# Optimization experiments

Hardware: AMD Instinct MI355X
Metric: run time of the kernel (lower is better)

Reference implementation:

```python
import jax, jax.numpy as jnp
import numpy as np

EPS = 1e-5

def _ln(t, g, b):
    m = t.mean(-1, keepdims=True)
    v = ((t - m) ** 2).mean(-1, keepdims=True)
    return (t - m) * jax.lax.rsqrt(v + EPS) * g + b

def _sr(t, w, b, H, W, sr):
    # t: [B, H*W, C] -> spatial-reduction conv -> [B, (H//sr)*(W//sr), C]
    B, L, C = t.shape
    xi = t.transpose(0, 2, 1).reshape(B, C, H, W)
    y = jax.lax.conv_general_dilated(xi, w, (sr, sr), 'VALID',
                                     dimension_numbers=('NCHW', 'OIHW', 'NCHW'))
    return y.reshape(B, C, -1).transpose(0, 2, 1) + b

def setup_inputs() -> dict:
    key = jax.random.key(0)
    ks = jax.random.split(key, 9)
    C, head, sr, H, W = 128, 2, 2, 64, 64
    B, N = 4, 2 * H * W
    s = 0.02
    return {
        'x': jax.random.normal(ks[0], (B, N, C), jnp.float32),
        'qW': jax.random.normal(ks[1], (C, C), jnp.float32) * s,
        'qb': jnp.zeros((C,), jnp.float32),
        'kvW': jax.random.normal(ks[2], (C, 2 * C), jnp.float32) * s,
        'kvb': jnp.zeros((2 * C,), jnp.float32),
        'projW': jax.random.normal(ks[3], (C, C), jnp.float32) * s,
        'projb': jnp.zeros((C,), jnp.float32),
        'srW': jax.random.normal(ks[4], (C, C, sr, sr), jnp.float32) * s,
        'srb': jnp.zeros((C,), jnp.float32),
        'lnW': jnp.ones((C,), jnp.float32),
        'lnB': jnp.zeros((C,), jnp.float32),
        'H': H, 'W': W, 'fuse': 1,
    }

def reference(x, qW, qb, kvW, kvb, projW, projb, srW, srb, lnW, lnB, H, W, fuse):
    head, sr = 2, 2
    B, N, C = x.shape
    Dh = C // head
    scale = Dh ** -0.5
    q = (x @ qW + qb).reshape(B, N, head, Dh).transpose(0, 2, 1, 3)  # [B,h,N,Dh]
    mask = None
    if fuse and sr > 1:
        half = N // 2
        x_rgb = _ln(_sr(x[:, :half, :], srW, srb, H, W, sr), lnW, lnB)
        x_dte = _ln(_sr(x[:, half:, :], srW, srb, H, W, sr), lnW, lnB)
        xkv = jnp.concatenate([x_rgb, x_dte], axis=1)
        M = N // (sr * sr)
        row = jnp.arange(N)[:, None] < half            # query in rgb half
        col = jnp.arange(M)[None, :] < (M // 2)        # key in rgb half
        mask = row == col                              # True on same-modality blocks -> masked
    elif sr > 1:
        xkv = _ln(_sr(x, srW, srb, H, W, sr), lnW, lnB)
    else:
        xkv = x
    M = xkv.shape[1]
    kv = (xkv @ kvW + kvb).reshape(B, M, 2, head, Dh).transpose(2, 0, 3, 1, 4)
    k, v = kv[0], kv[1]                                # [B,h,M,Dh]
    attn = jnp.einsum('bhnd,bhmd->bhnm', q, k) * scale
    if mask is not None:
        attn = jnp.where(mask[None, None], -jnp.inf, attn)
    attn = jax.nn.softmax(attn, axis=-1)
    out = jnp.einsum('bhnm,bhmd->bhnd', attn, v).transpose(0, 2, 1, 3).reshape(B, N, C)
    return out @ projW + projb
```

## Files before the change

kernel.cpp:

```cpp
#include <hip/hip_runtime.h>
#include <hip/hip_bf16.h>

#define LN_EPS 1e-5f

typedef __attribute__((ext_vector_type(8))) short bf16x8_t;
typedef __attribute__((ext_vector_type(4))) float f32x4_t;
typedef __attribute__((ext_vector_type(4))) unsigned short u16x4_t;

#define MFMA32(a, b, c) __builtin_amdgcn_mfma_f32_16x16x32_bf16(a, b, c, 0, 0, 0)

__device__ inline float fast_exp2(float x) {
#if __has_builtin(__builtin_amdgcn_exp2f)
    return __builtin_amdgcn_exp2f(x);
#else
    float r;
    asm volatile("v_exp_f32 %0, %1\n\ts_nop 0" : "=v"(r) : "v"(x));
    return r;
#endif
}

__device__ inline unsigned short f2bf(float f) {
    union { float f; unsigned int u; } v; v.f = f;
    unsigned int r = v.u + 0x7fffu + ((v.u >> 16) & 1u);
    return (unsigned short)(r >> 16);
}

__device__ inline u16x4_t pk4(float a, float b, float c, float d) {
    union { u16x4_t v; __hip_bfloat162 h[2]; } u;
    u.h[0] = __float22bfloat162_rn(float2{a, b});
    u.h[1] = __float22bfloat162_rn(float2{c, d});
    return u.v;
}
__device__ inline bf16x8_t pk8(float4 a, float4 b) {
    union { bf16x8_t v; __hip_bfloat162 h[4]; } u;
    u.h[0] = __float22bfloat162_rn(float2{a.x, a.y});
    u.h[1] = __float22bfloat162_rn(float2{a.z, a.w});
    u.h[2] = __float22bfloat162_rn(float2{b.x, b.y});
    u.h[3] = __float22bfloat162_rn(float2{b.z, b.w});
    return u.v;
}

__device__ inline size_t fragidx(int row, int k, int KC) {
    return ((size_t)((row >> 4) * KC + (k >> 5))) * 512 +
           (((k >> 3) & 3) * 16 + (row & 15)) * 8 + (k & 7);
}

__global__ void k_prep_w(const float* __restrict__ qW, const float* __restrict__ kvW,
                         const float* __restrict__ projW, const float* __restrict__ srW,
                         unsigned short* __restrict__ qWs, unsigned short* __restrict__ kvWs,
                         unsigned short* __restrict__ projWs, unsigned short* __restrict__ srWs) {
    int i = blockIdx.x * 256 + threadIdx.x;
    if (i < 16384) {
        int n = i & 127, k = i >> 7;
        qWs[fragidx(n, k, 4)] = f2bf(qW[k * 128 + n]);
    } else if (i < 49152) {
        int j = i - 16384; int n = j & 255, k = j >> 8;
        kvWs[fragidx(n, k, 4)] = f2bf(kvW[k * 256 + n]);
    } else if (i < 65536) {
        int j = i - 49152; int n = j & 127, k = j >> 7;
        projWs[fragidx(n, k, 4)] = f2bf(projW[k * 128 + n]);
    } else {
        int j = i - 65536; int n = j >> 9, rem = j & 511, q = rem >> 7, c = rem & 127;
        srWs[fragidx(n, q * 128 + c, 16)] = f2bf(srW[n * 512 + c * 4 + q]);
    }
}

#define XPAD 132
__global__ __launch_bounds__(256)
void k_convkv(const float* __restrict__ x, const unsigned short* __restrict__ srWs,
              const float* __restrict__ srb, const float* __restrict__ lnW,
              const float* __restrict__ lnB, const unsigned short* __restrict__ kvWs,
              const float* __restrict__ kvb, unsigned short* __restrict__ ksw,
              unsigned short* __restrict__ vls) {
    const int t = threadIdx.x, w = t >> 6, lane = t & 63;
    const int col = lane & 15, quad = lane >> 4;
    const int RT = blockIdx.x;

    __shared__ unsigned short xl[64 * XPAD];
    __shared__ unsigned short xs[4 * 512];
    __shared__ float lnred[4][16][2];

    const int pb = RT >> 7, phf = (RT >> 6) & 1;
    const int oy = (RT >> 1) & 31, ox0 = (RT & 1) * 16;
    const int n0 = phf * 4096 + 2 * oy * 64 + 2 * ox0;
    #pragma unroll
    for (int it = 0; it < 8; it++) {
        int idx = it * 256 + t;
        int chunk = idx >> 10;
        int rr = (idx >> 5) & 31;
        int c4 = idx & 31;
        float4 v = *(const float4*)(x + ((size_t)(pb * 8192 + n0 + chunk * 64 + rr)) * 128 + c4 * 4);
        *(u16x4_t*)(xl + (chunk * 32 + rr) * XPAD + c4 * 4) = pk4(v.x, v.y, v.z, v.w);
    }
    __syncthreads();

    f32x4_t acc[2] = {};
    {
        const unsigned short* wp = srWs + lane * 8;
        #pragma unroll
        for (int kc = 0; kc < 16; kc++) {
            const int q = kc >> 2, cg = kc & 3;
            const int r = (q >> 1) * 32 + 2 * col + (q & 1);
            bf16x8_t xb = *(const bf16x8_t*)(xl + r * XPAD + cg * 32 + quad * 8);
            #pragma unroll
            for (int jj = 0; jj < 2; jj++) {
                bf16x8_t wf = *(const bf16x8_t*)(wp + (size_t)((w * 2 + jj) * 16 + kc) * 512);
                acc[jj] = MFMA32(wf, xb, acc[jj]);
            }
        }
    }
    float s = 0.f, ss = 0.f;
    #pragma unroll
    for (int jj = 0; jj < 2; jj++) {
        float4 bs = *(const float4*)(srb + (w * 2 + jj) * 16 + quad * 4);
        acc[jj][0] += bs.x; acc[jj][1] += bs.y; acc[jj][2] += bs.z; acc[jj][3] += bs.w;
        #pragma unroll
        for (int r = 0; r < 4; r++) { float v = acc[jj][r]; s += v; ss += v * v; }
    }
    s += __shfl_xor(s, 16, 64);  s += __shfl_xor(s, 32, 64);
    ss += __shfl_xor(ss, 16, 64); ss += __shfl_xor(ss, 32, 64);
    if (lane < 16) { lnred[w][lane][0] = s; lnred[w][lane][1] = ss; }
    __syncthreads();
    float stot = 0.f, sstot = 0.f;
    #pragma unroll
    for (int ww = 0; ww < 4; ww++) { stot += lnred[ww][col][0]; sstot += lnred[ww][col][1]; }
    float mean = stot * (1.0f / 128.0f);
    float var = sstot * (1.0f / 128.0f) - mean * mean;
    float rs = rsqrtf(var + LN_EPS);
    #pragma unroll
    for (int jj = 0; jj < 2; jj++) {
        int f0 = (w * 2 + jj) * 16 + quad * 4;
        float4 g = *(const float4*)(lnW + f0);
        float4 be = *(const float4*)(lnB + f0);
        u16x4_t o = pk4((acc[jj][0] - mean) * rs * g.x + be.x,
                        (acc[jj][1] - mean) * rs * g.y + be.y,
                        (acc[jj][2] - mean) * rs * g.z + be.z,
                        (acc[jj][3] - mean) * rs * g.w + be.w);
        *(u16x4_t*)(xs + ((size_t)(f0 >> 5)) * 512 +
                    (((f0 >> 3) & 3) * 16 + col) * 8 + (f0 & 7)) = o;
    }
    __syncthreads();
    bf16x8_t xf[4];
    #pragma unroll
    for (int kc = 0; kc < 4; kc++)
        xf[kc] = *(const bf16x8_t*)(xs + (size_t)kc * 512 + lane * 8);
    const int p0 = RT * 16;
    const int bb = p0 >> 11;
    #pragma unroll
    for (int jj = 0; jj < 2; jj++) {
        const int nt = w * 2 + jj;
        f32x4_t aK = {};
        #pragma unroll
        for (int kc = 0; kc < 4; kc++) {
            bf16x8_t wf = *(const bf16x8_t*)(kvWs + (size_t)(nt * 4 + kc) * 512 + lane * 8);
            aK = MFMA32(wf, xf[kc], aK);
        }
        float4 bs = *(const float4*)(kvb + nt * 16 + quad * 4);
        int m = (p0 + col) & 2047;
        int bh = bb * 2 + (nt >> 2);
        int d0 = (nt & 3) * 16 + quad * 4;
        u16x4_t o = pk4(aK[0] + bs.x, aK[1] + bs.y, aK[2] + bs.z, aK[3] + bs.w);
        *(u16x4_t*)(ksw + ((size_t)(bh * 128 + (m >> 4)) * 2 + (d0 >> 5)) * 512 +
                    (((d0 >> 3) & 3) * 16 + (m & 15)) * 8 + (d0 & 7)) = o;
    }
    #pragma unroll
    for (int jj = 0; jj < 2; jj++) {
        const int nt = w * 2 + jj;
        f32x4_t aV = {};
        #pragma unroll
        for (int kc = 0; kc < 4; kc++) {
            bf16x8_t wf = *(const bf16x8_t*)(kvWs + (size_t)((8 + nt) * 4 + kc) * 512 + lane * 8);
            aV = MFMA32(xf[kc], wf, aV);
        }
        int fv = nt * 16 + col;
        int h = fv >> 6, dd = fv & 63;
        float bv = kvb[128 + fv];
        int m0 = (p0 + quad * 4) & 2047;
        int bh = bb * 2 + h;
        int kt = m0 >> 6;
        int tt = (m0 >> 5) & 1;
        int base = m0 & 31;
        int quad_b = base >> 3, j0 = base & 7;
        u16x4_t o = pk4(aV[0] + bv, aV[1] + bv, aV[2] + bv, aV[3] + bv);
        *(u16x4_t*)(vls + (((size_t)((bh * 32 + kt) * 4 + (dd >> 4)) * 2 + tt) * 512) +
                    (quad_b * 16 + (dd & 15)) * 8 + j0) = o;
    }
}

__global__ __launch_bounds__(256, 2)
void k_attn_f8(const float* __restrict__ x, const unsigned short* __restrict__ qWs,
               const float* __restrict__ qb, const unsigned short* __restrict__ ksw,
               const unsigned short* __restrict__ vls, const unsigned short* __restrict__ projWs,
               const float* __restrict__ projb, float* __restrict__ out) {
    const int blkx = blockIdx.x, mod = blockIdx.y, b = blockIdx.z;
    const int t = threadIdx.x, w = t >> 6, lane = t & 63;
    const int col = lane & 15, quad = lane >> 4;
    const int ks = w & 1, h = w >> 1;
    const int bh = b * 2 + h;
    const int qbase = mod * 4096 + blkx * 64;

    __shared__ unsigned short sbuf[64 * 136];
    __shared__ unsigned short pls[4][4096];
    __shared__ float Ocomb[64 * 68];
    __shared__ float lcomb[64];

    const float sc = 0.125f * 1.44269504089f;
    #pragma unroll
    for (int qtl = 0; qtl < 2; qtl++) {
        const int qt = ks * 2 + qtl;
        const float* xrow = x + ((size_t)b * 8192 + qbase + qt * 16 + col) * 128;
        f32x4_t acc[4] = {};
        #pragma unroll
        for (int kc = 0; kc < 4; kc++) {
            float4 xa = *(const float4*)(xrow + kc * 32 + quad * 8);
            float4 xb2 = *(const float4*)(xrow + kc * 32 + quad * 8 + 4);
            bf16x8_t xf = pk8(xa, xb2);
            #pragma unroll
            for (int j = 0; j < 4; j++) {
                bf16x8_t wf = *(const bf16x8_t*)(qWs + (size_t)((h * 4 + j) * 4 + kc) * 512 + lane * 8);
                acc[j] = MFMA32(wf, xf, acc[j]);
            }
        }
        #pragma unroll
        for (int j = 0; j < 4; j++) {
            float4 bs = *(const float4*)(qb + h * 64 + j * 16 + quad * 4);
            u16x4_t o = pk4((acc[j][0] + bs.x) * sc, (acc[j][1] + bs.y) * sc,
                            (acc[j][2] + bs.z) * sc, (acc[j][3] + bs.w) * sc);
            *(u16x4_t*)(sbuf + (size_t)h * 4096 + ((size_t)(qt * 2 + (j >> 1))) * 512 +
                        (((j & 1) * 2 + (quad >> 1)) * 16 + col) * 8 + (quad & 1) * 4) = o;
        }
    }
    __syncthreads();
    bf16x8_t qf[4][2];
    #pragma unroll
    for (int qt = 0; qt < 4; qt++)
        #pragma unroll
        for (int kc = 0; kc < 2; kc++)
            qf[qt][kc] = *(const bf16x8_t*)(sbuf + (size_t)h * 4096 +
                                            (size_t)(qt * 2 + kc) * 512 + lane * 8);
    __syncthreads();

    const unsigned short* kp0 =
        ksw + ((size_t)(bh * 128 + (1 - mod) * 64) * 2) * 512 + lane * 8;
    const unsigned short* vp0 =
        vls + ((size_t)((bh * 32 + (1 - mod) * 16) * 8)) * 512 + lane * 8;
    const bf16x8_t ones8 = { 0x3F80, 0x3F80, 0x3F80, 0x3F80,
                             0x3F80, 0x3F80, 0x3F80, 0x3F80 };
    unsigned short* parea = pls[w];

    f32x4_t O[4][4] = {};
    f32x4_t accl[4] = {};

    for (int kti = 0; kti < 8; kti++) {
        const int kt = ks * 8 + kti;
        bf16x8_t kf[8], vf[8];
        #pragma unroll
        for (int i = 0; i < 8; i++) {
            kf[i] = *(const bf16x8_t*)(kp0 + (size_t)(kt * 8 + i) * 512);
            vf[i] = *(const bf16x8_t*)(vp0 + (size_t)(kt * 8 + i) * 512);
        }
        #pragma unroll
        for (int qp = 0; qp < 2; qp++) {
            f32x4_t ST[2][4];
            #pragma unroll
            for (int qtl = 0; qtl < 2; qtl++) {
                const int qt = qp * 2 + qtl;
                #pragma unroll
                for (int nb = 0; nb < 4; nb++) {
                    f32x4_t sA = {};
                    sA = MFMA32(kf[nb * 2 + 0], qf[qt][0], sA);
                    sA = MFMA32(kf[nb * 2 + 1], qf[qt][1], sA);
                    ST[qtl][nb] = sA;
                }
            }
            #pragma unroll
            for (int qtl = 0; qtl < 2; qtl++)
                #pragma unroll
                for (int nb = 0; nb < 4; nb++) {
                    u16x4_t pk = pk4(fast_exp2(ST[qtl][nb][0]), fast_exp2(ST[qtl][nb][1]),
                                     fast_exp2(ST[qtl][nb][2]), fast_exp2(ST[qtl][nb][3]));
                    *(u16x4_t*)(parea + (qp * 2 + qtl) * 1024 + (nb >> 1) * 512 +
                                (((nb & 1) * 2 + (quad >> 1)) * 16 + col) * 8 + (quad & 1) * 4) = pk;
                }
            #pragma unroll
            for (int qtl = 0; qtl < 2; qtl++) {
                const int qt = qp * 2 + qtl;
                bf16x8_t pf0 = *(const bf16x8_t*)(parea + qt * 1024 + lane * 8);
                bf16x8_t pf1 = *(const bf16x8_t*)(parea + qt * 1024 + 512 + lane * 8);
                accl[qt] = MFMA32(pf0, ones8, accl[qt]);
                accl[qt] = MFMA32(pf1, ones8, accl[qt]);
                #pragma unroll
                for (int dt = 0; dt < 4; dt++) {
                    O[qt][dt] = MFMA32(pf0, vf[dt * 2 + 0], O[qt][dt]);
                    O[qt][dt] = MFMA32(pf1, vf[dt * 2 + 1], O[qt][dt]);
                }
            }
        }
    }

    #pragma unroll
    for (int hp = 0; hp < 2; hp++) {
        if (h == hp && ks == 1) {
            #pragma unroll
            for (int qt = 0; qt < 4; qt++)
                #pragma unroll
                for (int r = 0; r < 4; r++) {
                    int qrow = qt * 16 + quad * 4 + r;
                    #pragma unroll
                    for (int dt = 0; dt < 4; dt++)
                        Ocomb[qrow * 68 + dt * 16 + col] = O[qt][dt][r];
                    if (col == 0) lcomb[qrow] = accl[qt][r];
                }
        }
        __syncthreads();
        if (h == hp && ks == 0) {
            #pragma unroll
            for (int qt = 0; qt < 4; qt++)
                #pragma unroll
                for (int r = 0; r < 4; r++) {
                    int qrow = qt * 16 + quad * 4 + r;
                    float lt = accl[qt][r] + lcomb[qrow];
                    float rl = 1.0f / lt;
                    #pragma unroll
                    for (int dt = 0; dt < 4; dt++) {
                        float ov = O[qt][dt][r] + Ocomb[qrow * 68 + dt * 16 + col];
                        sbuf[qrow * 136 + hp * 64 + dt * 16 + col] = f2bf(ov * rl);
                    }
                }
        }
        __syncthreads();
    }

    {
        const int qt2 = w;
        bf16x8_t ob[4];
        #pragma unroll
        for (int kc = 0; kc < 4; kc++)
            ob[kc] = *(const bf16x8_t*)(sbuf + (size_t)(qt2 * 16 + col) * 136 + kc * 32 + quad * 8);
        f32x4_t acc[8];
        #pragma unroll
        for (int j = 0; j < 8; j++) acc[j] = f32x4_t{};
        #pragma unroll
        for (int kc = 0; kc < 4; kc++)
            #pragma unroll
            for (int j = 0; j < 8; j++) {
                bf16x8_t wf = *(const bf16x8_t*)(projWs + (size_t)(j * 4 + kc) * 512 + lane * 8);
                acc[j] = MFMA32(wf, ob[kc], acc[j]);
            }
        const int n = b * 8192 + qbase + qt2 * 16 + col;
        #pragma unroll
        for (int j = 0; j < 8; j++) {
            int f0 = j * 16 + quad * 4;
            float4 bs = *(const float4*)(projb + f0);
            float4 o = { acc[j][0] + bs.x, acc[j][1] + bs.y,
                         acc[j][2] + bs.z, acc[j][3] + bs.w };
            *(float4*)(out + (size_t)n * 128 + f0) = o;
        }
    }
}

extern "C" void kernel_launch(void* const* d_in, const int* in_sizes, int n_in,
                              void* d_out, int out_size, void* d_ws, size_t ws_size,
                              hipStream_t stream) {
    const float* x     = (const float*)d_in[0];
    const float* qW    = (const float*)d_in[1];
    const float* qb    = (const float*)d_in[2];
    const float* kvW   = (const float*)d_in[3];
    const float* kvb   = (const float*)d_in[4];
    const float* projW = (const float*)d_in[5];
    const float* projb = (const float*)d_in[6];
    const float* srW   = (const float*)d_in[7];
    const float* srb   = (const float*)d_in[8];
    const float* lnW   = (const float*)d_in[9];
    const float* lnB   = (const float*)d_in[10];

    char* ws = (char*)d_ws;
    unsigned short* qWs    = (unsigned short*)(ws + 0);
    unsigned short* kvWs   = (unsigned short*)(ws + 32768);
    unsigned short* projWs = (unsigned short*)(ws + 98304);
    unsigned short* srWs   = (unsigned short*)(ws + 131072);
    unsigned short* ksw    = (unsigned short*)(ws + 262144);
    unsigned short* vls    = (unsigned short*)(ws + 2359296);

    k_prep_w<<<dim3(512), dim3(256), 0, stream>>>(qW, kvW, projW, srW,
                                                  qWs, kvWs, projWs, srWs);
    k_convkv<<<dim3(512), dim3(256), 0, stream>>>(x, srWs, srb, lnW, lnB,
                                                  kvWs, kvb, ksw, vls);
    k_attn_f8<<<dim3(64, 2, 4), dim3(256), 0, stream>>>(x, qWs, qb, ksw, vls,
                                                        projWs, projb, (float*)d_out);
}
```

Before: 129.2 us.

## Alias shared memory into one arena and raise attention kernel occupancy

Replaces the separate shared buffers with one aliased arena. Q staging, per-wave P tiles (halved by reusing across query pairs) and output rows share space, roughly halving LDS per block. Launch bounds rise from 2 to 4 blocks per CU so more blocks can be resident. The tighter register budget risks spills, and an extra barrier is added to protect the aliased region.

```diff
diff --git a/kernel.cpp b/kernel.cpp
--- a/kernel.cpp
+++ b/kernel.cpp
@@ -187,8 +187,8 @@
     }
 }
 
-__global__ __launch_bounds__(256, 2)
-void k_attn_f8(const float* __restrict__ x, const unsigned short* __restrict__ qWs,
+__global__ __launch_bounds__(256, 4)
+void k_attn_f9(const float* __restrict__ x, const unsigned short* __restrict__ qWs,
                const float* __restrict__ qb, const unsigned short* __restrict__ ksw,
                const unsigned short* __restrict__ vls, const unsigned short* __restrict__ projWs,
                const float* __restrict__ projb, float* __restrict__ out) {
@@ -199,10 +199,12 @@
     const int bh = b * 2 + h;
     const int qbase = mod * 4096 + blkx * 64;
 
-    __shared__ unsigned short sbuf[64 * 136];
-    __shared__ unsigned short pls[4][4096];
-    __shared__ float Ocomb[64 * 68];
-    __shared__ float lcomb[64];
+    __shared__ char arena[35200];
+    unsigned short* qstage = (unsigned short*)arena;
+    unsigned short* pw     = (unsigned short*)arena + w * 2048;
+    unsigned short* rows   = (unsigned short*)arena;
+    float* Ocomb = (float*)(arena + 17536);
+    float* lcomb = (float*)(arena + 34944);
 
     const float sc = 0.125f * 1.44269504089f;
     #pragma unroll
@@ -226,7 +228,7 @@
             float4 bs = *(const float4*)(qb + h * 64 + j * 16 + quad * 4);
             u16x4_t o = pk4((acc[j][0] + bs.x) * sc, (acc[j][1] + bs.y) * sc,
                             (acc[j][2] + bs.z) * sc, (acc[j][3] + bs.w) * sc);
-            *(u16x4_t*)(sbuf + (size_t)h * 4096 + ((size_t)(qt * 2 + (j >> 1))) * 512 +
+            *(u16x4_t*)(qstage + (size_t)h * 4096 + ((size_t)(qt * 2 + (j >> 1))) * 512 +
                         (((j & 1) * 2 + (quad >> 1)) * 16 + col) * 8 + (quad & 1) * 4) = o;
         }
     }
@@ -236,7 +238,7 @@
     for (int qt = 0; qt < 4; qt++)
         #pragma unroll
         for (int kc = 0; kc < 2; kc++)
-            qf[qt][kc] = *(const bf16x8_t*)(sbuf + (size_t)h * 4096 +
+            qf[qt][kc] = *(const bf16x8_t*)(qstage + (size_t)h * 4096 +
                                             (size_t)(qt * 2 + kc) * 512 + lane * 8);
     __syncthreads();
 
@@ -246,7 +248,6 @@
         vls + ((size_t)((bh * 32 + (1 - mod) * 16) * 8)) * 512 + lane * 8;
     const bf16x8_t ones8 = { 0x3F80, 0x3F80, 0x3F80, 0x3F80,
                              0x3F80, 0x3F80, 0x3F80, 0x3F80 };
-    unsigned short* parea = pls[w];
 
     f32x4_t O[4][4] = {};
     f32x4_t accl[4] = {};
@@ -279,14 +280,14 @@
                 for (int nb = 0; nb < 4; nb++) {
                     u16x4_t pk = pk4(fast_exp2(ST[qtl][nb][0]), fast_exp2(ST[qtl][nb][1]),
                                      fast_exp2(ST[qtl][nb][2]), fast_exp2(ST[qtl][nb][3]));
-                    *(u16x4_t*)(parea + (qp * 2 + qtl) * 1024 + (nb >> 1) * 512 +
+                    *(u16x4_t*)(pw + qtl * 1024 + (nb >> 1) * 512 +
                                 (((nb & 1) * 2 + (quad >> 1)) * 16 + col) * 8 + (quad & 1) * 4) = pk;
                 }
             #pragma unroll
             for (int qtl = 0; qtl < 2; qtl++) {
                 const int qt = qp * 2 + qtl;
-                bf16x8_t pf0 = *(const bf16x8_t*)(parea + qt * 1024 + lane * 8);
-                bf16x8_t pf1 = *(const bf16x8_t*)(parea + qt * 1024 + 512 + lane * 8);
+                bf16x8_t pf0 = *(const bf16x8_t*)(pw + qtl * 1024 + lane * 8);
+                bf16x8_t pf1 = *(const bf16x8_t*)(pw + qtl * 1024 + 512 + lane * 8);
                 accl[qt] = MFMA32(pf0, ones8, accl[qt]);
                 accl[qt] = MFMA32(pf1, ones8, accl[qt]);
                 #pragma unroll
@@ -297,6 +298,7 @@
             }
         }
     }
+    __syncthreads();
 
     #pragma unroll
     for (int hp = 0; hp < 2; hp++) {
@@ -324,7 +326,7 @@
                     #pragma unroll
                     for (int dt = 0; dt < 4; dt++) {
                         float ov = O[qt][dt][r] + Ocomb[qrow * 68 + dt * 16 + col];
-                        sbuf[qrow * 136 + hp * 64 + dt * 16 + col] = f2bf(ov * rl);
+                        rows[qrow * 136 + hp * 64 + dt * 16 + col] = f2bf(ov * rl);
                     }
                 }
         }
@@ -336,7 +338,7 @@
         bf16x8_t ob[4];
         #pragma unroll
         for (int kc = 0; kc < 4; kc++)
-            ob[kc] = *(const bf16x8_t*)(sbuf + (size_t)(qt2 * 16 + col) * 136 + kc * 32 + quad * 8);
+            ob[kc] = *(const bf16x8_t*)(rows + (size_t)(qt2 * 16 + col) * 136 + kc * 32 + quad * 8);
         f32x4_t acc[8];
         #pragma unroll
         for (int j = 0; j < 8; j++) acc[j] = f32x4_t{};
@@ -386,6 +388,6 @@
                                                   qWs, kvWs, projWs, srWs);
     k_convkv<<<dim3(512), dim3(256), 0, stream>>>(x, srWs, srb, lnW, lnB,
                                                   kvWs, kvb, ksw, vls);
-    k_attn_f8<<<dim3(64, 2, 4), dim3(256), 0, stream>>>(x, qWs, qb, ksw, vls,
+    k_attn_f9<<<dim3(64, 2, 4), dim3(256), 0, stream>>>(x, qWs, qb, ksw, vls,
                                                         projWs, projb, (float*)d_out);
 }
```

After: 248.9 us. 92.7% more time.
